# Kernel tuning notes

Measured on AMD Instinct MI355X. Metric: run time of the kernel, lower is better.

## Reference

```python
import jax, jax.numpy as jnp
import numpy as np

STATE_DIM = 150
HIDDEN = 64
ACTION_DIM = 10
TEAM = 5
PRED_STEPS = 5
HEADS = 4
BATCH = 16384


def _lin_params(key, out_dim, in_dim):
    kw, kb = jax.random.split(key)
    w = jax.random.normal(kw, (out_dim, in_dim), dtype=jnp.float32) * 0.05
    b = jax.random.normal(kb, (out_dim,), dtype=jnp.float32) * 0.05
    return w, b


def setup_inputs() -> dict:
    key = jax.random.key(0)
    ks = jax.random.split(key, 16)
    x = jax.random.normal(ks[0], (BATCH, STATE_DIM), dtype=jnp.float32)
    fc1_w, fc1_b = _lin_params(ks[1], HIDDEN, STATE_DIM)
    fc2_w, fc2_b = _lin_params(ks[2], HIDDEN, HIDDEN)
    fc3_w, fc3_b = _lin_params(ks[3], ACTION_DIM, HIDDEN)
    h0_w, h0_b = _lin_params(ks[4], HIDDEN, HIDDEN)
    c0_w, c0_b = _lin_params(ks[5], HIDDEN, HIDDEN)
    lstm_wih = jax.random.normal(ks[6], (4 * HIDDEN, HIDDEN), dtype=jnp.float32) * 0.05
    lstm_whh = jax.random.normal(ks[7], (4 * HIDDEN, HIDDEN), dtype=jnp.float32) * 0.05
    lstm_bih = jax.random.normal(ks[8], (4 * HIDDEN,), dtype=jnp.float32) * 0.05
    lstm_bhh = jax.random.normal(ks[9], (4 * HIDDEN,), dtype=jnp.float32) * 0.05
    predfc_w, predfc_b = _lin_params(ks[10], TEAM * STATE_DIM, HIDDEN)
    emb_w, emb_b = _lin_params(ks[11], HIDDEN, STATE_DIM)
    attn_in_w = jax.random.normal(ks[12], (3 * HIDDEN, HIDDEN), dtype=jnp.float32) * 0.05
    attn_in_b = jax.random.normal(ks[13], (3 * HIDDEN,), dtype=jnp.float32) * 0.05
    attn_out_w, attn_out_b = _lin_params(ks[14], HIDDEN, HIDDEN)
    unemb_w, unemb_b = _lin_params(ks[15], STATE_DIM, HIDDEN)
    return dict(x=x, fc1_w=fc1_w, fc1_b=fc1_b, fc2_w=fc2_w, fc2_b=fc2_b,
                fc3_w=fc3_w, fc3_b=fc3_b, h0_w=h0_w, h0_b=h0_b, c0_w=c0_w,
                c0_b=c0_b, lstm_wih=lstm_wih, lstm_whh=lstm_whh,
                lstm_bih=lstm_bih, lstm_bhh=lstm_bhh, predfc_w=predfc_w,
                predfc_b=predfc_b, emb_w=emb_w, emb_b=emb_b,
                attn_in_w=attn_in_w, attn_in_b=attn_in_b,
                attn_out_w=attn_out_w, attn_out_b=attn_out_b,
                unemb_w=unemb_w, unemb_b=unemb_b)


def _mha(x, in_w, in_b, out_w, out_b):
    # x: [B, S, E]; torch MultiheadAttention with batch_first=True, q=k=v=x
    B, S, E = x.shape
    D = E // HEADS
    qkv = x @ in_w.T + in_b                      # [B, S, 3E]
    q, k, v = jnp.split(qkv, 3, axis=-1)
    def heads(t):  # [B, S, E] -> [B, H, S, D]
        return t.reshape(B, S, HEADS, D).transpose(0, 2, 1, 3)
    q, k, v = heads(q), heads(k), heads(v)
    scores = jnp.einsum('bhqd,bhkd->bhqk', q, k) / jnp.sqrt(jnp.float32(D))
    attn = jax.nn.softmax(scores, axis=-1)
    out = jnp.einsum('bhqk,bhkd->bhqd', attn, v)  # [B, H, S, D]
    out = out.transpose(0, 2, 1, 3).reshape(B, S, E)
    return out @ out_w.T + out_b


def reference(x, fc1_w, fc1_b, fc2_w, fc2_b, fc3_w, fc3_b, h0_w, h0_b, c0_w,
              c0_b, lstm_wih, lstm_whh, lstm_bih, lstm_bhh, predfc_w,
              predfc_b, emb_w, emb_b, attn_in_w, attn_in_b, attn_out_w,
              attn_out_b, unemb_w, unemb_b):
    B = x.shape[0]
    h1 = jax.nn.relu(x @ fc1_w.T + fc1_b)
    h2 = jax.nn.relu(h1 @ fc2_w.T + fc2_b)
    action_probs = jax.nn.softmax(h2 @ fc3_w.T + fc3_b, axis=1)
    h = h2 @ h0_w.T + h0_b
    c = h2 @ c0_w.T + c0_b
    zero_in = jnp.zeros((B, HIDDEN), dtype=x.dtype)

    def step(carry, _):
        h, c = carry
        gates = zero_in @ lstm_wih.T + lstm_bih + h @ lstm_whh.T + lstm_bhh
        i, f, g, o = jnp.split(gates, 4, axis=-1)
        c_new = jax.nn.sigmoid(f) * c + jax.nn.sigmoid(i) * jnp.tanh(g)
        h_new = jax.nn.sigmoid(o) * jnp.tanh(c_new)
        pred_step = (h_new @ predfc_w.T + predfc_b).reshape(B, TEAM, STATE_DIM)
        embeds = pred_step @ emb_w.T + emb_b          # [B, TEAM, HIDDEN]
        att = _mha(embeds, attn_in_w, attn_in_b, attn_out_w, attn_out_b)
        out = att @ unemb_w.T + unemb_b               # [B, TEAM, STATE_DIM]
        return (h_new, c_new), out

    (_, _), preds = jax.lax.scan(step, (h, c), None, length=PRED_STEPS)
    pred = preds.transpose(1, 0, 2, 3)  # [B, PRED_STEPS, TEAM, STATE_DIM]
    return action_probs, pred
```

## Files before the change

kernel.cpp:

```cpp
#include <hip/hip_runtime.h>


#define RF(x) __builtin_amdgcn_readfirstlane(x)

constexpr int BATCH = 16384;

typedef short bf16x8 __attribute__((ext_vector_type(8)));
typedef float f32x4  __attribute__((ext_vector_type(4)));

constexpr int WS_FC1T = 0;
constexpr int WS_FC2T = 9728;
constexpr int WS_FC3T = 13824;
constexpr int WS_H0T  = 14592;
constexpr int WS_C0T  = 18688;
constexpr int WS_WHHT = 22784;
constexpr int WS_GB   = 39168;
constexpr int WS_W2   = 39424;
constexpr int WS_B2   = 59904;
constexpr int WS_W3QK = 60224;
constexpr int WS_W3V  = 101184;
constexpr int WS_B3QK = 121664;
constexpr int WS_B3V  = 122304;
constexpr int WS_W4T  = 122624;
constexpr int WS_B4   = 132352;
constexpr int WS_FC3B = 132504;
constexpr int WS_W4F  = 132520;
constexpr int WS_GF   = 142760;
constexpr int WS_VF   = 159144;
constexpr int WS_QKF  = 179624;
constexpr int WS_TOTAL= 220584;

constexpr int VSTR     = 324;
constexpr int QK_OFF   = 10368;
constexpr int QKSTR    = 164;
constexpr int H_OFF    = 15616;
constexpr int C_OFF    = 17792;
constexpr int HSTR     = 68;
constexpr int XSTR     = 156;
constexpr int H1_OFF   = QK_OFF;
constexpr int H2_OFF   = 4992;
constexpr int LDS_DW   = 19968;

__device__ __forceinline__ unsigned rnbf16_bits(float f) {
    unsigned u = __float_as_uint(f);
    return (u + 0x7FFFu + ((u >> 16) & 1u)) >> 16;
}

__global__ void k_pre1(const float* __restrict__ fc1_w, const float* __restrict__ fc2_w,
                       const float* __restrict__ fc3_w, const float* __restrict__ fc3_b,
                       const float* __restrict__ h0_w,  const float* __restrict__ c0_w,
                       const float* __restrict__ whh,   const float* __restrict__ bih,
                       const float* __restrict__ bhh,
                       const float* __restrict__ predfc_w, const float* __restrict__ predfc_b,
                       const float* __restrict__ emb_w,    const float* __restrict__ emb_b,
                       const float* __restrict__ aow, const float* __restrict__ aob,
                       const float* __restrict__ unw, const float* __restrict__ unb,
                       float* ws)
{
    int idx = blockIdx.x * 256 + threadIdx.x;
    if (idx < 9728) { int k = idx / 64, c = idx & 63;
        ws[WS_FC1T + idx] = (k < 150) ? fc1_w[c * 150 + k] : 0.f; return; }
    idx -= 9728;
    if (idx < 4096) { int k = idx >> 6, c = idx & 63; ws[WS_FC2T + idx] = fc2_w[c * 64 + k]; return; }
    idx -= 4096;
    if (idx < 768)  { int k = idx / 12, c = idx % 12;
        ws[WS_FC3T + idx] = (c < 10) ? fc3_w[c * 64 + k] : 0.f; return; }
    idx -= 768;
    if (idx < 4096) { int k = idx >> 6, c = idx & 63; ws[WS_H0T + idx] = h0_w[c * 64 + k]; return; }
    idx -= 4096;
    if (idx < 4096) { int k = idx >> 6, c = idx & 63; ws[WS_C0T + idx] = c0_w[c * 64 + k]; return; }
    idx -= 4096;
    if (idx < 16384){ int k = idx >> 8, c = idx & 255; ws[WS_WHHT + idx] = whh[c * 64 + k]; return; }
    idx -= 16384;
    if (idx < 256)  { ws[WS_GB + idx] = bih[idx] + bhh[idx]; return; }
    idx -= 256;
    if (idx < 20480){ int t = idx / 4096, r = idx & 4095, kk = r >> 6, j = r & 63;
        float s = 0.f;
        for (int m = 0; m < 150; ++m)
            s = fmaf(emb_w[kk * 150 + m], predfc_w[(t * 150 + m) * 64 + j], s);
        ws[WS_W2 + idx] = s; return; }
    idx -= 20480;
    if (idx < 320)  { int t = idx / 64, kk = idx & 63;
        float s = emb_b[kk];
        for (int m = 0; m < 150; ++m)
            s = fmaf(emb_w[kk * 150 + m], predfc_b[t * 150 + m], s);
        ws[WS_B2 + idx] = s; return; }
    idx -= 320;
    if (idx < 9728) { int k = idx / 152, ss = idx % 152;
        float v = 0.f;
        if (ss < 150) { float a = 0.f;
            for (int kk = 0; kk < 64; ++kk) a = fmaf(unw[ss * 64 + kk], aow[kk * 64 + k], a);
            v = a; }
        ws[WS_W4T + idx] = v; return; }
    idx -= 9728;
    if (idx < 152)  { float v = 0.f;
        if (idx < 150) { float a = unb[idx];
            for (int kk = 0; kk < 64; ++kk) a = fmaf(unw[idx * 64 + kk], aob[kk], a);
            v = a; }
        ws[WS_B4 + idx] = v; return; }
    idx -= 152;
    if (idx < 12)   { ws[WS_FC3B + idx] = (idx < 10) ? fc3_b[idx] : 0.f; return; }
}
constexpr int PRE1_ITEMS = 70116;

__global__ void k_pre2(const float* __restrict__ aiw, const float* __restrict__ aib,
                       float* ws)
{
    int idx = blockIdx.x * 256 + threadIdx.x;
    const float* W2 = ws + WS_W2;
    const float* b2 = ws + WS_B2;
    if (idx < 40960) {
        int h = idx / 10240, r = idx % 10240, k = r / 160, c = r % 160;
        int t = c / 32, rr = c % 32;
        int row; float scale;
        if (rr < 16) { row = h * 16 + rr;            scale = 0.25f; }
        else         { row = 64 + h * 16 + (rr - 16); scale = 1.f;  }
        float s = 0.f;
        for (int kk = 0; kk < 64; ++kk)
            s = fmaf(aiw[row * 64 + kk], W2[t * 4096 + kk * 64 + k], s);
        ws[WS_W3QK + idx] = s * scale; return;
    }
    idx -= 40960;
    if (idx < 20480) {
        int k = idx / 320, c = idx % 320, t = c >> 6, r3 = c & 63;
        int row = 128 + r3;
        float s = 0.f;
        for (int kk = 0; kk < 64; ++kk)
            s = fmaf(aiw[row * 64 + kk], W2[t * 4096 + kk * 64 + k], s);
        ws[WS_W3V + idx] = s; return;
    }
    idx -= 20480;
    if (idx < 640) {
        int h = idx / 160, c = idx % 160, t = c / 32, rr = c % 32;
        int row; float scale;
        if (rr < 16) { row = h * 16 + rr;            scale = 0.25f; }
        else         { row = 64 + h * 16 + (rr - 16); scale = 1.f;  }
        float s = aib[row];
        for (int kk = 0; kk < 64; ++kk)
            s = fmaf(aiw[row * 64 + kk], b2[t * 64 + kk], s);
        ws[WS_B3QK + idx] = s * scale; return;
    }
    idx -= 640;
    if (idx < 320) {
        int t = idx >> 6, r3 = idx & 63, row = 128 + r3;
        float s = aib[row];
        for (int kk = 0; kk < 64; ++kk)
            s = fmaf(aiw[row * 64 + kk], b2[t * 64 + kk], s);
        ws[WS_B3V + idx] = s; return;
    }
}
constexpr int PRE2_ITEMS = 62400;

__global__ void k_pre3(float* ws)
{
    int idx = blockIdx.x * 256 + threadIdx.x;
    if (idx >= 10240) return;
    int j2 = idx & 3, l = (idx >> 2) & 63, r = idx >> 8;
    int split = r & 1, s = (r >> 1) & 1, n = r >> 2;
    int col = 16 * n + (l & 15);
    unsigned bits[2];
    #pragma unroll
    for (int q = 0; q < 2; ++q) {
        int k = 32 * s + 8 * (l >> 4) + 2 * j2 + q;
        float v = (col < 152) ? ws[WS_W4T + k * 152 + col] : 0.f;
        unsigned hb = rnbf16_bits(v);
        if (split == 0) bits[q] = hb;
        else {
            float fh = __uint_as_float(hb << 16);
            bits[q] = rnbf16_bits(v - fh);
        }
    }
    reinterpret_cast<unsigned*>(ws)[WS_W4F + idx] = bits[0] | (bits[1] << 16);
}

__global__ void k_pre4(float* ws)
{
    int idx = blockIdx.x * 256 + threadIdx.x;
    if (idx >= 77824) return;
    const float* src; int N, rel, dst;
    if (idx < 16384)      { src = ws + WS_WHHT; N = 256; rel = idx;         dst = WS_GF + idx; }
    else if (idx < 36864) { src = ws + WS_W3V;  N = 320; rel = idx - 16384; dst = WS_VF + rel; }
    else {
        int r = idx - 36864;
        int h = r / 10240;  rel = r % 10240;
        src = ws + WS_W3QK + h * 10240; N = 160;
        dst = WS_QKF + r;
    }
    int n = rel >> 10, sub = rel & 1023;
    int s = sub >> 9, split = (sub >> 8) & 1, lj = sub & 255;
    int l = lj >> 2, j2 = lj & 3;
    int col = n * 16 + (l & 15);
    unsigned bits[2];
    #pragma unroll
    for (int q = 0; q < 2; ++q) {
        int k = 32 * s + 8 * (l >> 4) + 2 * j2 + q;
        float v = src[k * N + col];
        unsigned hb = rnbf16_bits(v);
        if (split == 0) bits[q] = hb;
        else bits[q] = rnbf16_bits(v - __uint_as_float(hb << 16));
    }
    reinterpret_cast<unsigned*>(ws)[dst] = bits[0] | (bits[1] << 16);
}

__device__ __forceinline__ float sigf(float v) {
    return __builtin_amdgcn_rcpf(1.f + __expf(-v));
}
__device__ __forceinline__ float tanh_fast(float v) {
    float e = __expf(-2.f * v);
    return fmaf(-2.f, e * __builtin_amdgcn_rcpf(1.f + e), 1.f);
}

template<int NC, int K, int WS>
__device__ __forceinline__ void kloop(const float* __restrict__ wT,
                                      const float* __restrict__ a_row,
                                      float* acc)
{
    #pragma unroll 4
    for (int k = 0; k < K; k += 4) {
        const float4 av = *reinterpret_cast<const float4*>(a_row + k);
        const float* wr = wT + k * WS;
        #pragma unroll
        for (int c = 0; c < NC; ++c) acc[c] = fmaf(av.x, wr[c], acc[c]);
        #pragma unroll
        for (int c = 0; c < NC; ++c) acc[c] = fmaf(av.y, wr[WS + c], acc[c]);
        #pragma unroll
        for (int c = 0; c < NC; ++c) acc[c] = fmaf(av.z, wr[2 * WS + c], acc[c]);
        #pragma unroll
        for (int c = 0; c < NC; ++c) acc[c] = fmaf(av.w, wr[3 * WS + c], acc[c]);
    }
}

__device__ __forceinline__ f32x4 mfma_tile(const bf16x8* __restrict__ base,
                                           const bf16x8* ah, const bf16x8* al,
                                           int l, f32x4 acc)
{
    #pragma unroll
    for (int s = 0; s < 2; ++s) {
        bf16x8 bh = base[s * 128 + l];
        bf16x8 bl = base[s * 128 + 64 + l];
        acc = __builtin_amdgcn_mfma_f32_16x16x32_bf16(al[s], bh, acc, 0, 0, 0);
        acc = __builtin_amdgcn_mfma_f32_16x16x32_bf16(ah[s], bl, acc, 0, 0, 0);
        acc = __builtin_amdgcn_mfma_f32_16x16x32_bf16(ah[s], bh, acc, 0, 0, 0);
    }
    return acc;
}

__device__ __forceinline__ void build_afrag(const float* __restrict__ hbase,
                                            int m, int l, bf16x8* ah, bf16x8* al)
{
    const int arow = m * 16 + (l & 15);
    const int kb   = 8 * (l >> 4);
    #pragma unroll
    for (int s = 0; s < 2; ++s) {
        const float* ap = hbase + arow * HSTR + 32 * s + kb;
        float4 f0 = *reinterpret_cast<const float4*>(ap);
        float4 f1 = *reinterpret_cast<const float4*>(ap + 4);
        float fv[8] = {f0.x, f0.y, f0.z, f0.w, f1.x, f1.y, f1.z, f1.w};
        #pragma unroll
        for (int j = 0; j < 8; ++j) {
            unsigned hb = rnbf16_bits(fv[j]);
            ah[s][j] = (short)hb;
            al[s][j] = (short)rnbf16_bits(fv[j] - __uint_as_float(hb << 16));
        }
    }
}

__global__ void __launch_bounds__(512, 2)
policy_main(const float* __restrict__ x,
            const float* __restrict__ fc1_b, const float* __restrict__ fc2_b,
            const float* __restrict__ h0_b,  const float* __restrict__ c0_b,
            const float* __restrict__ ws,    float* __restrict__ out)
{
    __shared__ float lds[LDS_DW];

    const int tid = threadIdx.x;
    const int l   = tid & 63;
    const int w   = RF(tid >> 6);
    const int m   = w & 1;
    const int g   = w >> 1;
    const int el  = l & 31;
    const int hf  = l >> 5;
    const int e0  = blockIdx.x * 32;
    const int r0c = (l >> 4) << 2;

    for (int idx = tid; idx < 32 * XSTR; idx += 512) {
        int r = idx / XSTR, k = idx - r * XSTR;
        lds[idx] = (k < 150) ? x[(e0 + r) * 150 + k] : 0.f;
    }
    __syncthreads();

    {
        const int c0 = w * 8 + hf * 4;
        float acc[4];
        #pragma unroll
        for (int c = 0; c < 4; ++c) acc[c] = fc1_b[c0 + c];
        kloop<4, 152, 64>(ws + WS_FC1T + c0, lds + el * XSTR, acc);
        float* hp = lds + H1_OFF + el * HSTR + c0;
        *reinterpret_cast<float4*>(hp) =
            make_float4(fmaxf(acc[0],0.f), fmaxf(acc[1],0.f), fmaxf(acc[2],0.f), fmaxf(acc[3],0.f));
    }
    __syncthreads();

    {
        const int c0 = w * 8 + hf * 4;
        float acc[4];
        #pragma unroll
        for (int c = 0; c < 4; ++c) acc[c] = fc2_b[c0 + c];
        kloop<4, 64, 64>(ws + WS_FC2T + c0, lds + H1_OFF + el * HSTR, acc);
        float* hp = lds + H2_OFF + el * HSTR + c0;
        *reinterpret_cast<float4*>(hp) =
            make_float4(fmaxf(acc[0],0.f), fmaxf(acc[1],0.f), fmaxf(acc[2],0.f), fmaxf(acc[3],0.f));
    }
    __syncthreads();

    if (w == 0) {
        if (hf == 0) {
            float acc[12];
            #pragma unroll
            for (int c = 0; c < 12; ++c) acc[c] = ws[WS_FC3B + c];
            kloop<12, 64, 12>(ws + WS_FC3T, lds + H2_OFF + el * HSTR, acc);
            float mm = acc[0];
            #pragma unroll
            for (int i = 1; i < 10; ++i) mm = fmaxf(mm, acc[i]);
            float sum = 0.f;
            #pragma unroll
            for (int i = 0; i < 10; ++i) { acc[i] = __expf(acc[i] - mm); sum += acc[i]; }
            float inv = __builtin_amdgcn_rcpf(sum);
            float* op = out + (size_t)(e0 + el) * 10;
            #pragma unroll
            for (int i = 0; i < 10; i += 2)
                *reinterpret_cast<float2*>(op + i) = make_float2(acc[i] * inv, acc[i + 1] * inv);
        }
    } else {
        for (int j = w - 1; j < 16; j += 7) {
            const int  cc  = (j & 7) * 8 + hf * 4;
            const bool isC = (j >= 8);
            const float* wT = ws + (isC ? WS_C0T : WS_H0T) + cc;
            const float* bb = isC ? c0_b : h0_b;
            float acc[4];
            #pragma unroll
            for (int c = 0; c < 4; ++c) acc[c] = bb[cc + c];
            kloop<4, 64, 64>(wT, lds + H2_OFF + el * HSTR, acc);
            float* dp = lds + (isC ? C_OFF : H_OFF) + el * HSTR + cc;
            *reinterpret_cast<float4*>(dp) = make_float4(acc[0], acc[1], acc[2], acc[3]);
        }
    }
    __syncthreads();

    const bf16x8* gfrag  = reinterpret_cast<const bf16x8*>(ws + WS_GF);
    const bf16x8* vfrag  = reinterpret_cast<const bf16x8*>(ws + WS_VF);
    const bf16x8* qkfrag = reinterpret_cast<const bf16x8*>(ws + WS_QKF);

    const int grp  = tid >> 5;
    const int sel  = tid & 31;
    const int team = (grp < 5) ? grp : grp - 5;
    const int half = (grp < 5) ? 0 : 1;
    const int jcol = g * 16 + (l & 15);

    #pragma unroll 1
    for (int st = 0; st < 5; ++st) {
        {
            bf16x8 ah[2], al[2];
            build_afrag(lds + H_OFF, m, l, ah, al);
            f32x4 gacc[4];
            #pragma unroll 1
            for (int gi = 0; gi < 4; ++gi) {
                const int n = gi * 4 + g;
                float b = ws[WS_GB + gi * 64 + jcol];
                f32x4 acc = {b, b, b, b};
                gacc[gi] = mfma_tile(gfrag + n * 256, ah, al, l, acc);
            }
            #pragma unroll
            for (int q = 0; q < 4; ++q) {
                const int row = m * 16 + r0c + q;
                float c_ = lds[C_OFF + row * HSTR + jcol];
                float cc = sigf(gacc[1][q]) * c_ + sigf(gacc[0][q]) * tanh_fast(gacc[2][q]);
                float hn = sigf(gacc[3][q]) * tanh_fast(cc);
                lds[C_OFF + row * HSTR + jcol] = cc;
                lds[H_OFF + row * HSTR + jcol] = hn;
            }
        }
        __syncthreads();

        bf16x8 ah[2], al[2];
        build_afrag(lds + H_OFF, m, l, ah, al);
        {
            #pragma unroll 1
            for (int i = 0; i < 5; ++i) {
                const int n   = g * 5 + i;
                const int col = n * 16 + (l & 15);
                float b = ws[WS_B3V + col];
                f32x4 acc = {b, b, b, b};
                acc = mfma_tile(vfrag + n * 256, ah, al, l, acc);
                #pragma unroll
                for (int q = 0; q < 4; ++q)
                    lds[(m * 16 + r0c + q) * VSTR + col] = acc[q];
            }
            #pragma unroll 1
            for (int n = g; n < 10; n += 4) {
                const int col = n * 16 + (l & 15);
                float b = ws[WS_B3QK + col];
                f32x4 acc = {b, b, b, b};
                acc = mfma_tile(qkfrag + n * 256, ah, al, l, acc);
                #pragma unroll
                for (int q = 0; q < 4; ++q)
                    lds[QK_OFF + (m * 16 + r0c + q) * QKSTR + col] = acc[q];
            }
        }
        __syncthreads();

        float att[8];
        #pragma unroll 1
        for (int h = 0; h < 4; ++h) {
            if (tid < 320) {
                const float* qk = lds + QK_OFF + sel * QKSTR;
                float4 q0 = *reinterpret_cast<const float4*>(qk + team * 32);
                float4 q1 = *reinterpret_cast<const float4*>(qk + team * 32 + 4);
                float4 q2 = *reinterpret_cast<const float4*>(qk + team * 32 + 8);
                float4 q3 = *reinterpret_cast<const float4*>(qk + team * 32 + 12);
                float sc[5];
                #pragma unroll 2
                for (int t2 = 0; t2 < 5; ++t2) {
                    const float* kp = qk + t2 * 32 + 16;
                    float4 k0 = *reinterpret_cast<const float4*>(kp);
                    float4 k1 = *reinterpret_cast<const float4*>(kp + 4);
                    float4 k2 = *reinterpret_cast<const float4*>(kp + 8);
                    float4 k3 = *reinterpret_cast<const float4*>(kp + 12);
                    float d0 = q0.x * k0.x; d0 = fmaf(q0.y, k0.y, d0); d0 = fmaf(q0.z, k0.z, d0); d0 = fmaf(q0.w, k0.w, d0);
                    float d1 = q1.x * k1.x; d1 = fmaf(q1.y, k1.y, d1); d1 = fmaf(q1.z, k1.z, d1); d1 = fmaf(q1.w, k1.w, d1);
                    float d2 = q2.x * k2.x; d2 = fmaf(q2.y, k2.y, d2); d2 = fmaf(q2.z, k2.z, d2); d2 = fmaf(q2.w, k2.w, d2);
                    float d3 = q3.x * k3.x; d3 = fmaf(q3.y, k3.y, d3); d3 = fmaf(q3.z, k3.z, d3); d3 = fmaf(q3.w, k3.w, d3);
                    sc[t2] = (d0 + d1) + (d2 + d3);
                }
                float mm = fmaxf(fmaxf(fmaxf(sc[0], sc[1]), fmaxf(sc[2], sc[3])), sc[4]);
                float p[5];
                float sum = 0.f;
                #pragma unroll
                for (int t2 = 0; t2 < 5; ++t2) { p[t2] = __expf(sc[t2] - mm); sum += p[t2]; }
                float inv = __builtin_amdgcn_rcpf(sum);
                #pragma unroll
                for (int t2 = 0; t2 < 5; ++t2) p[t2] *= inv;

                #pragma unroll
                for (int r = 0; r < 8; ++r) att[r] = 0.f;
                const float* vr = lds + sel * VSTR + h * 16 + half * 8;
                #pragma unroll 2
                for (int t2 = 0; t2 < 5; ++t2) {
                    float4 v0 = *reinterpret_cast<const float4*>(vr + t2 * 64);
                    float4 v1 = *reinterpret_cast<const float4*>(vr + t2 * 64 + 4);
                    att[0] = fmaf(p[t2], v0.x, att[0]);
                    att[1] = fmaf(p[t2], v0.y, att[1]);
                    att[2] = fmaf(p[t2], v0.z, att[2]);
                    att[3] = fmaf(p[t2], v0.w, att[3]);
                    att[4] = fmaf(p[t2], v1.x, att[4]);
                    att[5] = fmaf(p[t2], v1.y, att[5]);
                    att[6] = fmaf(p[t2], v1.z, att[6]);
                    att[7] = fmaf(p[t2], v1.w, att[7]);
                }
            }
            __syncthreads();

            if (tid < 320) {
                float* ap = lds + sel * VSTR + team * 64 + h * 16 + half * 8;
                *reinterpret_cast<float4*>(ap)     = make_float4(att[0], att[1], att[2], att[3]);
                *reinterpret_cast<float4*>(ap + 4) = make_float4(att[4], att[5], att[6], att[7]);
            }
            if (h < 3) {
                #pragma unroll 1
                for (int n = g; n < 10; n += 4) {
                    const int col = n * 16 + (l & 15);
                    float b = ws[WS_B3QK + (h + 1) * 160 + col];
                    f32x4 acc = {b, b, b, b};
                    acc = mfma_tile(qkfrag + (h + 1) * 2560 + n * 256, ah, al, l, acc);
                    #pragma unroll
                    for (int q = 0; q < 4; ++q)
                        lds[QK_OFF + (m * 16 + r0c + q) * QKSTR + col] = acc[q];
                }
            }
            __syncthreads();
        }

        #pragma unroll 1
        for (int job = w; job < 10; job += 8) {
            const int t  = job >> 1;
            const int mj = job & 1;
            const int arow  = mj * 16 + (l & 15);
            const int kbase = 8 * (l >> 4);
            bf16x8 ah2[2], al2[2];
            #pragma unroll
            for (int s = 0; s < 2; ++s) {
                const float* ap = lds + arow * VSTR + t * 64 + 32 * s + kbase;
                float4 f0 = *reinterpret_cast<const float4*>(ap);
                float4 f1 = *reinterpret_cast<const float4*>(ap + 4);
                float fv[8] = {f0.x, f0.y, f0.z, f0.w, f1.x, f1.y, f1.z, f1.w};
                #pragma unroll
                for (int j = 0; j < 8; ++j) {
                    unsigned hb = rnbf16_bits(fv[j]);
                    float fh = __uint_as_float(hb << 16);
                    ah2[s][j] = (short)hb;
                    al2[s][j] = (short)rnbf16_bits(fv[j] - fh);
                }
            }
            const bf16x8* wb = reinterpret_cast<const bf16x8*>(ws + WS_W4F);
            const int cl = l & 15;
            #pragma unroll 1
            for (int n = 0; n < 10; ++n) {
                const int c = n * 16 + cl;
                float bias = ws[WS_B4 + (c < 151 ? c : 151)];
                f32x4 acc = {bias, bias, bias, bias};
                acc = mfma_tile(wb + n * 256, ah2, al2, l, acc);
                if (c < 150) {
                    const int r0 = mj * 16 + r0c;
                    #pragma unroll
                    for (int q = 0; q < 4; ++q)
                        out[(size_t)BATCH * 10 +
                            ((size_t)((e0 + r0 + q) * 5 + st) * 5 + t) * 150 + c] = acc[q];
                }
            }
        }
        __syncthreads();
    }
}

extern "C" void kernel_launch(void* const* d_in, const int* in_sizes, int n_in,
                              void* d_out, int out_size, void* d_ws, size_t ws_size,
                              hipStream_t stream)
{
    const float* x        = (const float*)d_in[0];
    const float* fc1_w    = (const float*)d_in[1];
    const float* fc1_b    = (const float*)d_in[2];
    const float* fc2_w    = (const float*)d_in[3];
    const float* fc2_b    = (const float*)d_in[4];
    const float* fc3_w    = (const float*)d_in[5];
    const float* fc3_b    = (const float*)d_in[6];
    const float* h0_w     = (const float*)d_in[7];
    const float* h0_b     = (const float*)d_in[8];
    const float* c0_w     = (const float*)d_in[9];
    const float* c0_b     = (const float*)d_in[10];
    const float* lstm_whh = (const float*)d_in[12];
    const float* lstm_bih = (const float*)d_in[13];
    const float* lstm_bhh = (const float*)d_in[14];
    const float* predfc_w = (const float*)d_in[15];
    const float* predfc_b = (const float*)d_in[16];
    const float* emb_w    = (const float*)d_in[17];
    const float* emb_b    = (const float*)d_in[18];
    const float* attn_in_w= (const float*)d_in[19];
    const float* attn_in_b= (const float*)d_in[20];
    const float* attn_out_w=(const float*)d_in[21];
    const float* attn_out_b=(const float*)d_in[22];
    const float* unemb_w  = (const float*)d_in[23];
    const float* unemb_b  = (const float*)d_in[24];

    float* ws  = (float*)d_ws;
    float* outp= (float*)d_out;

    k_pre1<<<(PRE1_ITEMS + 255) / 256, 256, 0, stream>>>(
        fc1_w, fc2_w, fc3_w, fc3_b, h0_w, c0_w,
        lstm_whh, lstm_bih, lstm_bhh,
        predfc_w, predfc_b, emb_w, emb_b,
        attn_out_w, attn_out_b, unemb_w, unemb_b, ws);

    k_pre2<<<(PRE2_ITEMS + 255) / 256, 256, 0, stream>>>(attn_in_w, attn_in_b, ws);

    k_pre3<<<40, 256, 0, stream>>>(ws);
    k_pre4<<<304, 256, 0, stream>>>(ws);

    policy_main<<<BATCH / 32, 512, 0, stream>>>(
        x, fc1_b, fc2_b, h0_b, c0_b, ws, outp);
}
```

Baseline: 228.0 us.

## Defer unembed stage into next step's gate phase and split jobs finer

The unembed (attention output to state) MFMA stage is moved out of the end of each step and run at the start of the next step, before the LSTM gate MFMAs, with one final call after the loop. This removes one barrier per step and lets the unembed work overlap with the gate computation. The unembed work is also split into 20 jobs instead of 10, so all 8 waves share the load more evenly. To keep the attention buffer intact until it is consumed, a barrier is added between the gate MFMAs and the LDS writes of the cell state.

```diff
diff --git a/kernel.cpp b/kernel.cpp
--- a/kernel.cpp
+++ b/kernel.cpp
@@ -282,6 +282,8 @@
     const int hf  = l >> 5;
     const int e0  = blockIdx.x * 32;
     const int r0c = (l >> 4) << 2;
+    const int cl16 = l & 15;
+    const int kb   = 8 * (l >> 4);
 
     for (int idx = tid; idx < 32 * XSTR; idx += 512) {
         int r = idx / XSTR, k = idx - r * XSTR;
@@ -350,19 +352,61 @@
     const bf16x8* gfrag  = reinterpret_cast<const bf16x8*>(ws + WS_GF);
     const bf16x8* vfrag  = reinterpret_cast<const bf16x8*>(ws + WS_VF);
     const bf16x8* qkfrag = reinterpret_cast<const bf16x8*>(ws + WS_QKF);
+    const bf16x8* wb     = reinterpret_cast<const bf16x8*>(ws + WS_W4F);
 
     const int grp  = tid >> 5;
     const int sel  = tid & 31;
     const int team = (grp < 5) ? grp : grp - 5;
     const int half = (grp < 5) ? 0 : 1;
-    const int jcol = g * 16 + (l & 15);
+    const int jcol = g * 16 + cl16;
+
+    auto do_s7 = [&](int sst) {
+        #pragma unroll 1
+        for (int job = w; job < 20; job += 8) {
+            const int t  = job >> 2;
+            const int mj = (job >> 1) & 1;
+            const int nh = job & 1;
+            const int arow = mj * 16 + cl16;
+            bf16x8 ah2[2], al2[2];
+            #pragma unroll
+            for (int s = 0; s < 2; ++s) {
+                const float* ap = lds + arow * VSTR + t * 64 + 32 * s + kb;
+                float4 f0 = *reinterpret_cast<const float4*>(ap);
+                float4 f1 = *reinterpret_cast<const float4*>(ap + 4);
+                float fv[8] = {f0.x, f0.y, f0.z, f0.w, f1.x, f1.y, f1.z, f1.w};
+                #pragma unroll
+                for (int j = 0; j < 8; ++j) {
+                    unsigned hb = rnbf16_bits(fv[j]);
+                    float fh = __uint_as_float(hb << 16);
+                    ah2[s][j] = (short)hb;
+                    al2[s][j] = (short)rnbf16_bits(fv[j] - fh);
+                }
+            }
+            #pragma unroll 1
+            for (int i = 0; i < 5; ++i) {
+                const int n = nh * 5 + i;
+                const int c = n * 16 + cl16;
+                float bias = ws[WS_B4 + (c < 151 ? c : 151)];
+                f32x4 acc = {bias, bias, bias, bias};
+                acc = mfma_tile(wb + n * 256, ah2, al2, l, acc);
+                if (c < 150) {
+                    const int r0 = mj * 16 + r0c;
+                    #pragma unroll
+                    for (int q = 0; q < 4; ++q)
+                        out[(size_t)BATCH * 10 +
+                            ((size_t)((e0 + r0 + q) * 5 + sst) * 5 + t) * 150 + c] = acc[q];
+                }
+            }
+        }
+    };
 
     #pragma unroll 1
     for (int st = 0; st < 5; ++st) {
+        f32x4 gacc[4];
         {
+            if (st > 0) do_s7(st - 1);
             bf16x8 ah[2], al[2];
             build_afrag(lds + H_OFF, m, l, ah, al);
-            f32x4 gacc[4];
             #pragma unroll 1
             for (int gi = 0; gi < 4; ++gi) {
                 const int n = gi * 4 + g;
@@ -370,6 +414,10 @@
                 f32x4 acc = {b, b, b, b};
                 gacc[gi] = mfma_tile(gfrag + n * 256, ah, al, l, acc);
             }
+        }
+        __syncthreads();
+
+        {
             #pragma unroll
             for (int q = 0; q < 4; ++q) {
                 const int row = m * 16 + r0c + q;
@@ -388,7 +436,7 @@
             #pragma unroll 1
             for (int i = 0; i < 5; ++i) {
                 const int n   = g * 5 + i;
-                const int col = n * 16 + (l & 15);
+                const int col = n * 16 + cl16;
                 float b = ws[WS_B3V + col];
                 f32x4 acc = {b, b, b, b};
                 acc = mfma_tile(vfrag + n * 256, ah, al, l, acc);
@@ -398,7 +446,7 @@
             }
             #pragma unroll 1
             for (int n = g; n < 10; n += 4) {
-                const int col = n * 16 + (l & 15);
+                const int col = n * 16 + cl16;
                 float b = ws[WS_B3QK + col];
                 f32x4 acc = {b, b, b, b};
                 acc = mfma_tile(qkfrag + n * 256, ah, al, l, acc);
@@ -468,7 +516,7 @@
             if (h < 3) {
                 #pragma unroll 1
                 for (int n = g; n < 10; n += 4) {
-                    const int col = n * 16 + (l & 15);
+                    const int col = n * 16 + cl16;
                     float b = ws[WS_B3QK + (h + 1) * 160 + col];
                     f32x4 acc = {b, b, b, b};
                     acc = mfma_tile(qkfrag + (h + 1) * 2560 + n * 256, ah, al, l, acc);
@@ -479,47 +527,9 @@
             }
             __syncthreads();
         }
-
-        #pragma unroll 1
-        for (int job = w; job < 10; job += 8) {
-            const int t  = job >> 1;
-            const int mj = job & 1;
-            const int arow  = mj * 16 + (l & 15);
-            const int kbase = 8 * (l >> 4);
-            bf16x8 ah2[2], al2[2];
-            #pragma unroll
-            for (int s = 0; s < 2; ++s) {
-                const float* ap = lds + arow * VSTR + t * 64 + 32 * s + kbase;
-                float4 f0 = *reinterpret_cast<const float4*>(ap);
-                float4 f1 = *reinterpret_cast<const float4*>(ap + 4);
-                float fv[8] = {f0.x, f0.y, f0.z, f0.w, f1.x, f1.y, f1.z, f1.w};
-                #pragma unroll
-                for (int j = 0; j < 8; ++j) {
-                    unsigned hb = rnbf16_bits(fv[j]);
-                    float fh = __uint_as_float(hb << 16);
-                    ah2[s][j] = (short)hb;
-                    al2[s][j] = (short)rnbf16_bits(fv[j] - fh);
-                }
-            }
-            const bf16x8* wb = reinterpret_cast<const bf16x8*>(ws + WS_W4F);
-            const int cl = l & 15;
-            #pragma unroll 1
-            for (int n = 0; n < 10; ++n) {
-                const int c = n * 16 + cl;
-                float bias = ws[WS_B4 + (c < 151 ? c : 151)];
-                f32x4 acc = {bias, bias, bias, bias};
-                acc = mfma_tile(wb + n * 256, ah2, al2, l, acc);
-                if (c < 150) {
-                    const int r0 = mj * 16 + r0c;
-                    #pragma unroll
-                    for (int q = 0; q < 4; ++q)
-                        out[(size_t)BATCH * 10 +
-                            ((size_t)((e0 + r0 + q) * 5 + st) * 5 + t) * 150 + c] = acc[q];
-                }
-            }
-        }
-        __syncthreads();
-    }
+    }
+
+    do_s7(4);
 }
 
 extern "C" void kernel_launch(void* const* d_in, const int* in_sizes, int n_in,
```

Measured after the change: 331.0 us. +45.1%, slower.
